# Optimization experiments

Hardware: AMD Instinct MI355X
Metric: run time of the kernel (lower is better)

## Reference

```python
import jax, jax.numpy as jnp
import numpy as np

B, N, F, T = 64, 1024, 8, 12
H, NLAYERS, K, OUT = 32, 3, 10, 12
E_RAND = N * 32


def setup_inputs() -> dict:
    key = jax.random.key(0)
    ks = jax.random.split(key, 11)
    x = jax.random.normal(ks[0], (B, N, F, T), jnp.float32)
    src = jax.random.randint(ks[1], (E_RAND,), 0, N)
    dst = jax.random.randint(ks[2], (E_RAND,), 0, N)
    loop = jnp.arange(N)
    edge_index = jnp.stack([jnp.concatenate([src, loop]),
                            jnp.concatenate([dst, loop])]).astype(jnp.int32)
    # weights in (0.1, 1.0) so all degrees are strictly positive
    edge_weight = jax.random.uniform(ks[3], (E_RAND + N,), jnp.float32, 0.1, 1.0)
    s = 0.1  # ~ 1/sqrt(H) init scale, matches torch defaults in spirit
    gru_w_ih = jax.random.normal(ks[4], (3 * H, F), jnp.float32) * s
    gru_w_hh = jax.random.normal(ks[5], (3 * H, H), jnp.float32) * s
    gru_b_ih = jax.random.normal(ks[6], (3 * H,), jnp.float32) * s
    gru_b_hh = jax.random.normal(ks[7], (3 * H,), jnp.float32) * s
    conv_w = jax.random.normal(ks[8], (NLAYERS, H, H), jnp.float32) * (1.0 / np.sqrt(H))
    lin_w = jax.random.normal(ks[9], (H, OUT), jnp.float32) * (1.0 / np.sqrt(H))
    lin_b = jax.random.normal(ks[10], (OUT,), jnp.float32) * s
    return {"x": x, "edge_index": edge_index, "edge_weight": edge_weight,
            "gru_w_ih": gru_w_ih, "gru_w_hh": gru_w_hh,
            "gru_b_ih": gru_b_ih, "gru_b_hh": gru_b_hh,
            "conv_w": conv_w, "lin_w": lin_w, "lin_b": lin_b}


def reference(x, edge_index, edge_weight, gru_w_ih, gru_w_hh, gru_b_ih, gru_b_hh,
              conv_w, lin_w, lin_b):
    Bsz, Nn, Fe, Tt = x.shape
    Hh = gru_w_hh.shape[1]

    # ---- temporal GRU over [B*N, T, F], keep last hidden state ----
    xt = jnp.transpose(x, (0, 1, 3, 2)).reshape(Bsz * Nn, Tt, Fe)
    gates_x = xt @ gru_w_ih.T + gru_b_ih  # [BN, T, 3H], input gates precomputed

    def step(h, gx):
        gh = h @ gru_w_hh.T + gru_b_hh
        xr, xz, xn = jnp.split(gx, 3, axis=-1)
        hr, hz, hn = jnp.split(gh, 3, axis=-1)
        r = jax.nn.sigmoid(xr + hr)
        z = jax.nn.sigmoid(xz + hz)
        n = jnp.tanh(xn + r * hn)
        return (1.0 - z) * n + z * h, None

    h0 = jnp.zeros((Bsz * Nn, Hh), x.dtype)
    hT, _ = jax.lax.scan(step, h0, jnp.swapaxes(gates_x, 0, 1))
    h = hT.reshape(Bsz, Nn, Hh)  # [B, N, H]

    # ---- normalized Laplacian (shared across batch) ----
    A = jnp.zeros((Nn, Nn), x.dtype).at[edge_index[0], edge_index[1]].add(edge_weight)
    d_isqrt = 1.0 / jnp.sqrt(A.sum(axis=1))  # row-degree, matches A.sum(dim=2)
    Lap = jnp.eye(Nn, dtype=x.dtype) - d_isqrt[:, None] * A * d_isqrt[None, :]

    # ---- rank-K spectral filter: M = U_k diag(S_k) U_k^T ----
    # torch code SVDs the identical L[b] per batch element; sign flips of U
    # columns cancel in U_k (.) U_k^T, so one SVD is mathematically identical.
    U, S, _ = jnp.linalg.svd(Lap, full_matrices=False)
    M = (U[:, :K] * S[:K]) @ U[:, :K].T  # [N, N]

    for w in conv_w:  # static 3-layer loop
        h = jax.nn.relu(jnp.einsum('nm,bmh,hk->bnk', M, h, w)) + h

    return h @ lin_w + lin_b  # [B, N, 12]
```

## Files before the change

### kernel.cpp

```cpp
#include <hip/hip_runtime.h>
#include <math.h>


#define NN 1024
#define PP 48
#define JSWEEPS 3

__global__ __launch_bounds__(256) void k_gru(
    const float* __restrict__ x, const float* __restrict__ wih,
    const float* __restrict__ whh, const float* __restrict__ bih,
    const float* __restrict__ bhh, float* __restrict__ hout) {
  __shared__ float s_x[64][97];
  __shared__ float s_h[64][33];
  int tid = threadIdx.x;
  int row = tid & 63;
  int i_base = __builtin_amdgcn_readfirstlane((tid >> 6) * 8);
  long row0 = (long)blockIdx.x * 64;

  for (int i = tid; i < 64 * 24; i += 256) {
    int r = i / 24, c = i % 24;
    float4 v = *(const float4*)&x[(row0 + r) * 96 + c * 4];
    s_x[r][c * 4 + 0] = v.x; s_x[r][c * 4 + 1] = v.y;
    s_x[r][c * 4 + 2] = v.z; s_x[r][c * 4 + 3] = v.w;
  }
  for (int i = tid; i < 64 * 32; i += 256) s_h[i / 32][i % 32] = 0.f;
  __syncthreads();

  float h[32];
#pragma unroll
  for (int k = 0; k < 32; ++k) h[k] = 0.f;

  for (int t = 0; t < 12; ++t) {
    float x8[8];
#pragma unroll
    for (int f = 0; f < 8; ++f) x8[f] = s_x[row][f * 12 + t];
    for (int ii = 0; ii < 8; ++ii) {
      int i = i_base + ii;
      float ar = bih[i] + bhh[i];
      float az = bih[32 + i] + bhh[32 + i];
      float gx = bih[64 + i];
      float gh = bhh[64 + i];
#pragma unroll
      for (int f = 0; f < 8; ++f) {
        ar += x8[f] * wih[i * 8 + f];
        az += x8[f] * wih[(32 + i) * 8 + f];
        gx += x8[f] * wih[(64 + i) * 8 + f];
      }
#pragma unroll
      for (int k = 0; k < 32; ++k) {
        ar += h[k] * whh[i * 32 + k];
        az += h[k] * whh[(32 + i) * 32 + k];
        gh += h[k] * whh[(64 + i) * 32 + k];
      }
      ar = fminf(fmaxf(ar, -30.f), 30.f);
      az = fminf(fmaxf(az, -30.f), 30.f);
      float r = __frcp_rn(1.f + __expf(-ar));
      float z = __frcp_rn(1.f + __expf(-az));
      float a = gx + r * gh;
      a = fminf(fmaxf(a, -15.f), 15.f);
      float e2 = __expf(2.f * a);
      float n = (e2 - 1.f) * __frcp_rn(e2 + 1.f);
      float hold = s_h[row][i];
      s_h[row][i] = (1.f - z) * n + z * hold;
    }
    __syncthreads();
#pragma unroll
    for (int k = 0; k < 32; ++k) h[k] = s_h[row][k];
    __syncthreads();
  }
  for (int idx = tid; idx < 64 * 8; idx += 256) {
    int r = idx >> 3, c4 = idx & 7;
    float4 v = make_float4(s_h[r][c4 * 4], s_h[r][c4 * 4 + 1],
                           s_h[r][c4 * 4 + 2], s_h[r][c4 * 4 + 3]);
    *(float4*)&hout[(row0 + r) * 32 + c4 * 4] = v;
  }
}

__global__ void k_scatter(const int* __restrict__ ei, const float* __restrict__ ew,
                          float* __restrict__ A, int E) {
  int e = blockIdx.x * 256 + threadIdx.x;
  if (e < E) atomicAdd(&A[ei[e] * NN + ei[E + e]], ew[e]);
}

__global__ __launch_bounds__(256) void k_degree(const float* __restrict__ A,
                                                float* __restrict__ disq) {
  __shared__ float red[256];
  int row = blockIdx.x, tid = threadIdx.x;
  float s = 0.f;
  for (int j = tid; j < NN; j += 256) s += A[row * NN + j];
  red[tid] = s;
  __syncthreads();
  for (int off = 128; off > 0; off >>= 1) {
    if (tid < off) red[tid] += red[tid + off];
    __syncthreads();
  }
  if (tid == 0) disq[row] = 1.f / sqrtf(red[0]);
}

__global__ void k_lap(float* __restrict__ A, const float* __restrict__ disq) {
  int idx = blockIdx.x * 256 + threadIdx.x;
  int i = idx >> 10, j = idx & 1023;
  float v = -disq[i] * A[idx] * disq[j];
  if (i == j) v += 1.f;
  A[idx] = v;
}

__global__ __launch_bounds__(256) void k_mm_sym(const float* __restrict__ A,
                                                float* __restrict__ C) {
  if (blockIdx.x < blockIdx.y) return;
  __shared__ float As[32][68];
  __shared__ float Bs[32][68];
  __shared__ float Ts[64][65];
  int tid = threadIdx.x;
  int tx = tid & 15, ty = tid >> 4;
  int i0 = blockIdx.y * 64, j0 = blockIdx.x * 64;
  float acc[4][4];
#pragma unroll
  for (int a = 0; a < 4; ++a)
#pragma unroll
    for (int b = 0; b < 4; ++b) acc[a][b] = 0.f;
  int lrow = tid >> 3;
  int kk0 = (tid & 7) * 4;
  float4 pa0 = *(const float4*)&A[(long)(i0 + lrow) * NN + kk0];
  float4 pa1 = *(const float4*)&A[(long)(i0 + lrow + 32) * NN + kk0];
  float4 pb0 = *(const float4*)&A[(long)(j0 + lrow) * NN + kk0];
  float4 pb1 = *(const float4*)&A[(long)(j0 + lrow + 32) * NN + kk0];
  for (int k0 = 0; k0 < NN; k0 += 32) {
    As[kk0 + 0][lrow] = pa0.x; As[kk0 + 1][lrow] = pa0.y;
    As[kk0 + 2][lrow] = pa0.z; As[kk0 + 3][lrow] = pa0.w;
    As[kk0 + 0][lrow + 32] = pa1.x; As[kk0 + 1][lrow + 32] = pa1.y;
    As[kk0 + 2][lrow + 32] = pa1.z; As[kk0 + 3][lrow + 32] = pa1.w;
    Bs[kk0 + 0][lrow] = pb0.x; Bs[kk0 + 1][lrow] = pb0.y;
    Bs[kk0 + 2][lrow] = pb0.z; Bs[kk0 + 3][lrow] = pb0.w;
    Bs[kk0 + 0][lrow + 32] = pb1.x; Bs[kk0 + 1][lrow + 32] = pb1.y;
    Bs[kk0 + 2][lrow + 32] = pb1.z; Bs[kk0 + 3][lrow + 32] = pb1.w;
    __syncthreads();
    if (k0 + 32 < NN) {
      pa0 = *(const float4*)&A[(long)(i0 + lrow) * NN + k0 + 32 + kk0];
      pa1 = *(const float4*)&A[(long)(i0 + lrow + 32) * NN + k0 + 32 + kk0];
      pb0 = *(const float4*)&A[(long)(j0 + lrow) * NN + k0 + 32 + kk0];
      pb1 = *(const float4*)&A[(long)(j0 + lrow + 32) * NN + k0 + 32 + kk0];
    }
#pragma unroll
    for (int kk = 0; kk < 32; ++kk) {
      float4 av = *(const float4*)&As[kk][ty * 4];
      float4 bv = *(const float4*)&Bs[kk][tx * 4];
      float aa[4] = {av.x, av.y, av.z, av.w};
      float bb[4] = {bv.x, bv.y, bv.z, bv.w};
#pragma unroll
      for (int a = 0; a < 4; ++a)
#pragma unroll
        for (int b = 0; b < 4; ++b) acc[a][b] += aa[a] * bb[b];
    }
    __syncthreads();
  }
#pragma unroll
  for (int a = 0; a < 4; ++a) {
    float4 v = make_float4(acc[a][0], acc[a][1], acc[a][2], acc[a][3]);
    *(float4*)&C[(long)(i0 + ty * 4 + a) * NN + j0 + tx * 4] = v;
  }
  if (i0 != j0) {
#pragma unroll
    for (int a = 0; a < 4; ++a)
#pragma unroll
      for (int b = 0; b < 4; ++b)
        Ts[tx * 4 + b][ty * 4 + a] = acc[a][b];
    __syncthreads();
    for (int idx = tid; idx < 64 * 16; idx += 256) {
      int r = idx >> 4, c4 = idx & 15;
      float4 v = make_float4(Ts[r][c4 * 4], Ts[r][c4 * 4 + 1],
                             Ts[r][c4 * 4 + 2], Ts[r][c4 * 4 + 3]);
      *(float4*)&C[(long)(j0 + r) * NN + i0 + c4 * 4] = v;
    }
  }
}

__global__ void k_q0(float* __restrict__ Q) {
  int i = blockIdx.x * 256 + threadIdx.x;
  if (i < NN * PP) {
    unsigned u = (unsigned)i * 2654435761u;
    u ^= u >> 16; u *= 2246822519u; u ^= u >> 13; u *= 3266489917u; u ^= u >> 16;
    Q[i] = (float)(u & 0xFFFFFF) * (1.f / 16777216.f) - 0.5f;
  }
}

__global__ __launch_bounds__(256) void k_spmm(const float* __restrict__ Gp,
                                              const float* __restrict__ Q,
                                              float* __restrict__ Zp) {
  __shared__ float Qs[64][49];
  __shared__ float Gs[16][65];
  int tid = threadIdx.x;
  int r = tid >> 4;
  int c0 = (tid & 15) * 3;
  int row0 = blockIdx.x * 16;
  int k0 = blockIdx.y * 256;
  float a0 = 0.f, a1 = 0.f, a2 = 0.f;
  for (int kt = 0; kt < 4; ++kt) {
    int kb = k0 + kt * 64;
    for (int idx = tid; idx < 64 * PP; idx += 256) {
      int qr = idx / PP, qc = idx % PP;
      Qs[qr][qc] = Q[(kb + qr) * PP + qc];
    }
    for (int idx = tid; idx < 16 * 64; idx += 256) {
      int gr = idx >> 6, gk = idx & 63;
      Gs[gr][gk] = Gp[(long)(row0 + gr) * NN + kb + gk];
    }
    __syncthreads();
#pragma unroll 4
    for (int kk = 0; kk < 64; ++kk) {
      float g = Gs[r][kk];
      a0 += g * Qs[kk][c0];
      a1 += g * Qs[kk][c0 + 1];
      a2 += g * Qs[kk][c0 + 2];
    }
    __syncthreads();
  }
  float* zp = Zp + (long)blockIdx.y * (NN * PP);
  zp[(row0 + r) * PP + c0] = a0;
  zp[(row0 + r) * PP + c0 + 1] = a1;
  zp[(row0 + r) * PP + c0 + 2] = a2;
}

__global__ __launch_bounds__(256) void k_gram(const float* __restrict__ Zp,
                                              float* __restrict__ Z,
                                              float* __restrict__ Sp) {
  __shared__ float Zs[32][49];
  int tid = threadIdx.x;
  int r0 = blockIdx.x * 32;
  for (int idx = tid; idx < 32 * PP; idx += 256) {
    int r = idx / PP, c = idx % PP;
    long g = (long)(r0 + r) * PP + c;
    float s = Zp[g] + Zp[g + NN * PP] + Zp[g + 2 * NN * PP] + Zp[g + 3 * NN * PP];
    Zs[r][c] = s;
    Z[g] = s;
  }
  __syncthreads();
  float* sp = Sp + blockIdx.x * (PP * PP);
  for (int cell = tid; cell < PP * PP; cell += 256) {
    int i = cell / PP, j = cell % PP;
    float a = 0.f;
#pragma unroll 8
    for (int r = 0; r < 32; ++r) a += Zs[r][i] * Zs[r][j];
    sp[cell] = a;
  }
}

__global__ __launch_bounds__(256) void k_tbuild(const float* __restrict__ Qa,
                                                const float* __restrict__ Zp,
                                                float* __restrict__ Tp) {
  __shared__ float Qs[32][49];
  __shared__ float Ys[32][49];
  int tid = threadIdx.x;
  int r0 = blockIdx.x * 32;
  for (int idx = tid; idx < 32 * PP; idx += 256) {
    int r = idx / PP, c = idx % PP;
    long g = (long)(r0 + r) * PP + c;
    Qs[r][c] = Qa[g];
    Ys[r][c] = Zp[g] + Zp[g + NN * PP] + Zp[g + 2 * NN * PP] + Zp[g + 3 * NN * PP];
  }
  __syncthreads();
  float* tp = Tp + blockIdx.x * (PP * PP);
  for (int cell = tid; cell < PP * PP; cell += 256) {
    int i = cell / PP, j = cell % PP;
    float a = 0.f;
#pragma unroll 8
    for (int r = 0; r < 32; ++r) a += Qs[r][i] * Ys[r][j];
    tp[cell] = a;
  }
}

__global__ __launch_bounds__(256) void k_qr(const float* __restrict__ Sp,
                                            float* __restrict__ Q) {
  __shared__ float R[PP][PP + 1];
  __shared__ float rs[PP];
  __shared__ float idiag[PP];
  int tid = threadIdx.x;
  for (int idx = tid; idx < PP * PP; idx += 256) {
    float s = 0.f;
    for (int b = 0; b < 32; ++b) s += Sp[b * (PP * PP) + idx];
    R[idx / PP][idx % PP] = s;
  }
  __syncthreads();
  for (int j = 0; j < PP; ++j) {
    float d = R[j][j];
    float sq = sqrtf(d > 1e-30f ? d : 1e-30f);
    float invd = 1.f / sq;
    for (int c = j + tid; c < PP; c += 256)
      rs[c] = (c == j) ? sq : R[j][c] * invd;
    __syncthreads();
    int m = PP - 1 - j;
    for (int idx = tid; idx < m * m; idx += 256) {
      int i = j + 1 + idx / m, c = j + 1 + idx % m;
      R[i][c] -= rs[i] * rs[c];
    }
    for (int c = j + tid; c < PP; c += 256) R[j][c] = rs[c];
    __syncthreads();
  }
  if (tid < PP) idiag[tid] = 1.f / R[tid][tid];
  __syncthreads();
  int row = blockIdx.x * 256 + tid;
  float q[PP];
#pragma unroll
  for (int k = 0; k < PP; ++k) q[k] = Q[row * PP + k];
#pragma unroll
  for (int c = 0; c < PP; ++c) {
    float s = q[c];
#pragma unroll
    for (int k = 0; k < c; ++k) s -= q[k] * R[k][c];
    q[c] = s * idiag[c];
  }
#pragma unroll
  for (int k = 0; k < PP; ++k) Q[row * PP + k] = q[k];
}

__global__ __launch_bounds__(384) void k_jacobi(const float* __restrict__ Tp,
                                                float* __restrict__ Vsel,
                                                float* __restrict__ s10) {
  __shared__ float Ta[PP][PP + 1], Tb[PP][PP + 1];
  __shared__ float Va[PP][PP + 1], Vb[PP][PP + 1];
  __shared__ float w0[PP], w1[PP];
  __shared__ int j0a[PP], j1a[PP];
  __shared__ int selidx[10];
  int tid = threadIdx.x;
  for (int idx = tid; idx < PP * PP; idx += 384) {
    float s = 0.f;
    for (int b = 0; b < 32; ++b) s += Tp[b * (PP * PP) + idx];
    Tb[idx / PP][idx % PP] = s;
  }
  __syncthreads();
  for (int idx = tid; idx < PP * PP; idx += 384) {
    int i = idx / PP, j = idx % PP;
    Ta[i][j] = 0.5f * (Tb[i][j] + Tb[j][i]);
    Va[i][j] = (i == j) ? 1.f : 0.f;
  }
  __syncthreads();
  float (*Tc)[PP + 1] = Ta, (*Tn)[PP + 1] = Tb;
  float (*Vc)[PP + 1] = Va, (*Vn)[PP + 1] = Vb;
  int i_row = tid >> 3;
  int jb = (tid & 7) * 6;
  for (int sweep = 0; sweep < JSWEEPS; ++sweep) {
    for (int r = 0; r < PP - 1; ++r) {
      if (tid < 24) {
        int k = tid;
        int p = (k == 0) ? 0 : ((r + k - 1) % 47) + 1;
        int q = ((r + 46 - k) % 47) + 1;
        float app = Tc[p][p], aqq = Tc[q][q], apq = Tc[p][q];
        float c = 1.f, s = 0.f;
        if (fabsf(apq) > 1e-30f) {
          float tau = (aqq - app) / (2.f * apq);
          float den = fabsf(tau) + sqrtf(1.f + tau * tau);
          float tt = copysignf(1.f / den, tau);
          c = 1.f / sqrtf(1.f + tt * tt);
          s = tt * c;
        }
        j0a[p] = p; j1a[p] = q; w0[p] = c;  w1[p] = -s;
        j0a[q] = p; j1a[q] = q; w0[q] = s;  w1[q] = c;
      }
      __syncthreads();
      float wi0 = w0[i_row], wi1 = w1[i_row];
      int i0 = j0a[i_row], i1 = j1a[i_row];
      float tnew[6], vnew[6];
#pragma unroll
      for (int m = 0; m < 6; ++m) {
        int j = jb + m;
        float wj0 = w0[j], wj1 = w1[j];
        int a = j0a[j], b = j1a[j];
        tnew[m] = wi0 * (wj0 * Tc[i0][a] + wj1 * Tc[i0][b]) +
                  wi1 * (wj0 * Tc[i1][a] + wj1 * Tc[i1][b]);
        vnew[m] = wj0 * Vc[i_row][a] + wj1 * Vc[i_row][b];
      }
#pragma unroll
      for (int m = 0; m < 6; ++m) {
        Tn[i_row][jb + m] = tnew[m];
        Vn[i_row][jb + m] = vnew[m];
      }
      __syncthreads();
      float (*tt_)[PP + 1] = Tc; Tc = Tn; Tn = tt_;
      float (*vt_)[PP + 1] = Vc; Vc = Vn; Vn = vt_;
    }
  }
  if (tid < 64) {
    float v = (tid < PP) ? Tc[tid][tid] : -1e30f;
    for (int sel = 0; sel < 10; ++sel) {
      float bv = v; int bi = tid;
      for (int off = 32; off > 0; off >>= 1) {
        float ov = __shfl_xor(bv, off);
        int oi = __shfl_xor(bi, off);
        if (ov > bv || (ov == bv && oi < bi)) { bv = ov; bi = oi; }
      }
      if (tid == 0) { selidx[sel] = bi; s10[sel] = sqrtf(fmaxf(bv, 0.f)); }
      if (tid == bi) v = -1e30f;
    }
  }
  __syncthreads();
  for (int idx = tid; idx < PP * 10; idx += 384) {
    int j = idx / 10, i = idx % 10;
    Vsel[idx] = Vc[j][selidx[i]];
  }
}

__global__ __launch_bounds__(256) void k_u10(const float* __restrict__ Q,
                                             const float* __restrict__ Vsel,
                                             float* __restrict__ U10) {
  __shared__ float Vs[PP * 10];
  int tid = threadIdx.x;
  for (int idx = tid; idx < PP * 10; idx += 256) Vs[idx] = Vsel[idx];
  __syncthreads();
  int row = blockIdx.x * 256 + tid;
  float q[PP];
#pragma unroll
  for (int k = 0; k < PP; ++k) q[k] = Q[row * PP + k];
#pragma unroll
  for (int i = 0; i < 10; ++i) {
    float s = 0.f;
#pragma unroll
    for (int k = 0; k < PP; ++k) s += q[k] * Vs[k * 10 + i];
    U10[row * 10 + i] = s;
  }
}

__global__ __launch_bounds__(320) void k_p0w(const float* __restrict__ h,
                                             const float* __restrict__ U10,
                                             const float* __restrict__ W,
                                             const float* __restrict__ s10,
                                             float* __restrict__ P1) {
  __shared__ float Hs[128][33];
  __shared__ float Us[128][10];
  __shared__ float P0s[10][33];
  __shared__ float Ws[32][32];
  int tid = threadIdx.x;
  int b = blockIdx.x;
  int i = tid / 32, kk = tid % 32;
  for (int idx = tid; idx < 1024; idx += 320) Ws[idx / 32][idx % 32] = W[idx];
  float acc = 0.f;
  for (int t0 = 0; t0 < NN; t0 += 128) {
    for (int idx = tid; idx < 128 * 32; idx += 320) {
      int r = idx / 32, c = idx % 32;
      Hs[r][c] = h[(long)(b * NN + t0 + r) * 32 + c];
    }
    for (int idx = tid; idx < 1280; idx += 320)
      Us[idx / 10][idx % 10] = U10[(t0 + idx / 10) * 10 + idx % 10];
    __syncthreads();
#pragma unroll 8
    for (int r = 0; r < 128; ++r) acc += Us[r][i] * Hs[r][kk];
    __syncthreads();
  }
  P0s[i][kk] = acc;
  __syncthreads();
  float a = 0.f;
#pragma unroll
  for (int j = 0; j < 32; ++j) a += P0s[i][j] * Ws[j][kk];
  P1[b * 320 + i * 32 + kk] = s10[i] * a;
}

template <int LAST>
__global__ __launch_bounds__(256) void k_update(float* __restrict__ h,
                                                const float* __restrict__ U10,
                                                const float* __restrict__ P1,
                                                const float* __restrict__ lw,
                                                const float* __restrict__ lb,
                                                float* __restrict__ out) {
  __shared__ float a1[10][32];
  __shared__ float Us[64][10];
  __shared__ float hl[64][33];
  int tid = threadIdx.x;
  int b = blockIdx.x, n0 = blockIdx.y * 64;
  for (int idx = tid; idx < 320; idx += 256)
    a1[idx / 32][idx % 32] = P1[b * 320 + idx];
  for (int idx = tid; idx < 640; idx += 256)
    Us[idx / 10][idx % 10] = U10[(n0 + idx / 10) * 10 + idx % 10];
  __syncthreads();
  for (int idx = tid; idx < 2048; idx += 256) {
    int nl = idx / 32, k = idx % 32;
    float z = 0.f;
#pragma unroll
    for (int i = 0; i < 10; ++i) z += Us[nl][i] * a1[i][k];
    long g = (long)(b * NN + n0 + nl) * 32 + k;
    float hn = h[g] + fmaxf(z, 0.f);
    if (LAST) hl[nl][k] = hn;
    else h[g] = hn;
  }
  if (LAST) {
    __syncthreads();
    for (int idx = tid; idx < 64 * 12; idx += 256) {
      int row = idx / 12, o = idx % 12;
      float s = lb[o];
#pragma unroll
      for (int j = 0; j < 32; ++j) s += hl[row][j] * lw[j * 12 + o];
      out[(long)(b * NN + n0 + row) * 12 + o] = s;
    }
  }
}

extern "C" void kernel_launch(void* const* d_in, const int* in_sizes, int n_in,
                              void* d_out, int out_size, void* d_ws, size_t ws_size,
                              hipStream_t stream) {
  const float* x    = (const float*)d_in[0];
  const int*   ei   = (const int*)d_in[1];
  const float* ew   = (const float*)d_in[2];
  const float* wih  = (const float*)d_in[3];
  const float* whh  = (const float*)d_in[4];
  const float* bih  = (const float*)d_in[5];
  const float* bhh  = (const float*)d_in[6];
  const float* convw = (const float*)d_in[7];
  const float* lw   = (const float*)d_in[8];
  const float* lb   = (const float*)d_in[9];
  float* out = (float*)d_out;
  float* ws  = (float*)d_ws;
  int E = in_sizes[1] / 2;

  float* h    = ws;
  float* B1   = h + 2097152;
  float* B2   = B1 + 1048576;
  float* B3   = B2 + 1048576;
  float* Qa   = B3 + 1048576;
  float* Qb   = Qa + 49152;
  float* Zp   = Qb + 49152;
  float* Sp   = Zp + 196608;
  float* Tp   = Sp + 73728;
  float* Vsel = Tp + 73728;
  float* s10  = Vsel + 480;
  float* U10  = s10 + 16;
  float* P1   = U10 + 10240;
  float* disq = P1 + 20480;

  k_gru<<<1024, 256, 0, stream>>>(x, wih, whh, bih, bhh, h);

  hipMemsetAsync(B1, 0, (size_t)1048576 * 4, stream);
  k_scatter<<<(E + 255) / 256, 256, 0, stream>>>(ei, ew, B1, E);
  k_degree<<<NN, 256, 0, stream>>>(B1, disq);
  k_lap<<<4096, 256, 0, stream>>>(B1, disq);
  k_mm_sym<<<dim3(16, 16), 256, 0, stream>>>(B1, B2);
  k_mm_sym<<<dim3(16, 16), 256, 0, stream>>>(B2, B3);
  k_mm_sym<<<dim3(16, 16), 256, 0, stream>>>(B3, B1);
  k_mm_sym<<<dim3(16, 16), 256, 0, stream>>>(B1, B3);
  k_mm_sym<<<dim3(16, 16), 256, 0, stream>>>(B3, B1);
  k_mm_sym<<<dim3(16, 16), 256, 0, stream>>>(B1, B3);

  k_q0<<<192, 256, 0, stream>>>(Qa);
  for (int it = 0; it < 6; ++it) {
    float* src = (it & 1) ? Qb : Qa;
    float* dst = (it & 1) ? Qa : Qb;
    k_spmm<<<dim3(64, 4), 256, 0, stream>>>(B3, src, Zp);
    k_gram<<<32, 256, 0, stream>>>(Zp, dst, Sp);
    k_qr<<<4, 256, 0, stream>>>(Sp, dst);
  }

  k_spmm<<<dim3(64, 4), 256, 0, stream>>>(B2, Qa, Zp);
  k_tbuild<<<32, 256, 0, stream>>>(Qa, Zp, Tp);
  k_jacobi<<<1, 384, 0, stream>>>(Tp, Vsel, s10);
  k_u10<<<4, 256, 0, stream>>>(Qa, Vsel, U10);

  for (int l = 0; l < 3; ++l) {
    k_p0w<<<64, 320, 0, stream>>>(h, U10, convw + l * 1024, s10, P1);
    if (l < 2)
      k_update<0><<<dim3(64, 16), 256, 0, stream>>>(h, U10, P1, lw, lb, out);
    else
      k_update<1><<<dim3(64, 16), 256, 0, stream>>>(h, U10, P1, lw, lb, out);
  }
}
```

Before: 1.270 ms.

## Split-K matrix powers, fuse Laplacian build, pipeline Jacobi coefficients, split P0 reduction

The symmetric 1024x1024 matrix-power products drop the half-grid triangle trick and run as a full grid with a two-way split over K, followed by a fold kernel. This raises block count from 136 active to 512. The Laplacian normalisation moves into the first product's tile load, which removes the separate k_lap pass. The single-block Jacobi eigensolver adds a warp that computes the next round's rotation coefficients while the other threads apply the current rotation, halving the barriers per round. The per-layer U^T h reduction is split across four blocks per batch element, with the W multiply moved into the update kernel. The GRU launch moves after the spectral stage so the h buffer can serve as split-K scratch. The costs are extra global traffic for the partials and the fold, and redundant W multiplies in every update block.

Result: faster. 1.130 ms (-11.1%).

```diff
diff --git a/kernel.cpp b/kernel.cpp
--- a/kernel.cpp
+++ b/kernel.cpp
@@ -5,6 +5,7 @@
 #define NN 1024
 #define PP 48
 #define JSWEEPS 3
+#define NROUNDS (JSWEEPS * (PP - 1))
 
 __global__ __launch_bounds__(256) void k_gru(
     const float* __restrict__ x, const float* __restrict__ wih,
@@ -97,23 +98,16 @@
   if (tid == 0) disq[row] = 1.f / sqrtf(red[0]);
 }
 
-__global__ void k_lap(float* __restrict__ A, const float* __restrict__ disq) {
-  int idx = blockIdx.x * 256 + threadIdx.x;
-  int i = idx >> 10, j = idx & 1023;
-  float v = -disq[i] * A[idx] * disq[j];
-  if (i == j) v += 1.f;
-  A[idx] = v;
-}
-
-__global__ __launch_bounds__(256) void k_mm_sym(const float* __restrict__ A,
-                                                float* __restrict__ C) {
-  if (blockIdx.x < blockIdx.y) return;
+template <int LAP>
+__global__ __launch_bounds__(256) void k_mmsplit(const float* __restrict__ A,
+                                                 const float* __restrict__ disq,
+                                                 float* __restrict__ Cp) {
   __shared__ float As[32][68];
   __shared__ float Bs[32][68];
-  __shared__ float Ts[64][65];
   int tid = threadIdx.x;
   int tx = tid & 15, ty = tid >> 4;
   int i0 = blockIdx.y * 64, j0 = blockIdx.x * 64;
+  int kbase = blockIdx.z * 512;
   float acc[4][4];
 #pragma unroll
   for (int a = 0; a < 4; ++a)
@@ -121,21 +115,43 @@
     for (int b = 0; b < 4; ++b) acc[a][b] = 0.f;
   int lrow = tid >> 3;
   int kk0 = (tid & 7) * 4;
-  float4 pa0 = *(const float4*)&A[(long)(i0 + lrow) * NN + kk0];
-  float4 pa1 = *(const float4*)&A[(long)(i0 + lrow + 32) * NN + kk0];
-  float4 pb0 = *(const float4*)&A[(long)(j0 + lrow) * NN + kk0];
-  float4 pb1 = *(const float4*)&A[(long)(j0 + lrow + 32) * NN + kk0];
-  for (int k0 = 0; k0 < NN; k0 += 32) {
-    As[kk0 + 0][lrow] = pa0.x; As[kk0 + 1][lrow] = pa0.y;
-    As[kk0 + 2][lrow] = pa0.z; As[kk0 + 3][lrow] = pa0.w;
-    As[kk0 + 0][lrow + 32] = pa1.x; As[kk0 + 1][lrow + 32] = pa1.y;
-    As[kk0 + 2][lrow + 32] = pa1.z; As[kk0 + 3][lrow + 32] = pa1.w;
-    Bs[kk0 + 0][lrow] = pb0.x; Bs[kk0 + 1][lrow] = pb0.y;
-    Bs[kk0 + 2][lrow] = pb0.z; Bs[kk0 + 3][lrow] = pb0.w;
-    Bs[kk0 + 0][lrow + 32] = pb1.x; Bs[kk0 + 1][lrow + 32] = pb1.y;
-    Bs[kk0 + 2][lrow + 32] = pb1.z; Bs[kk0 + 3][lrow + 32] = pb1.w;
-    __syncthreads();
-    if (k0 + 32 < NN) {
+  float drA0 = 0.f, drA1 = 0.f, drB0 = 0.f, drB1 = 0.f;
+  if (LAP) {
+    drA0 = disq[i0 + lrow]; drA1 = disq[i0 + lrow + 32];
+    drB0 = disq[j0 + lrow]; drB1 = disq[j0 + lrow + 32];
+  }
+  float4 pa0 = *(const float4*)&A[(long)(i0 + lrow) * NN + kbase + kk0];
+  float4 pa1 = *(const float4*)&A[(long)(i0 + lrow + 32) * NN + kbase + kk0];
+  float4 pb0 = *(const float4*)&A[(long)(j0 + lrow) * NN + kbase + kk0];
+  float4 pb1 = *(const float4*)&A[(long)(j0 + lrow + 32) * NN + kbase + kk0];
+  for (int k0 = kbase; k0 < kbase + 512; k0 += 32) {
+    if (LAP) {
+      float4 dq = *(const float4*)&disq[k0 + kk0];
+      int kg = k0 + kk0;
+#pragma unroll
+      for (int e = 0; e < 4; ++e) {
+        float dqe = (e == 0) ? dq.x : (e == 1) ? dq.y : (e == 2) ? dq.z : dq.w;
+        float a0e = (e == 0) ? pa0.x : (e == 1) ? pa0.y : (e == 2) ? pa0.z : pa0.w;
+        float a1e = (e == 0) ? pa1.x : (e == 1) ? pa1.y : (e == 2) ? pa1.z : pa1.w;
+        float b0e = (e == 0) ? pb0.x : (e == 1) ? pb0.y : (e == 2) ? pb0.z : pb0.w;
+        float b1e = (e == 0) ? pb1.x : (e == 1) ? pb1.y : (e == 2) ? pb1.z : pb1.w;
+        As[kk0 + e][lrow]      = -drA0 * a0e * dqe + ((i0 + lrow == kg + e) ? 1.f : 0.f);
+        As[kk0 + e][lrow + 32] = -drA1 * a1e * dqe + ((i0 + lrow + 32 == kg + e) ? 1.f : 0.f);
+        Bs[kk0 + e][lrow]      = -drB0 * b0e * dqe + ((j0 + lrow == kg + e) ? 1.f : 0.f);
+        Bs[kk0 + e][lrow + 32] = -drB1 * b1e * dqe + ((j0 + lrow + 32 == kg + e) ? 1.f : 0.f);
+      }
+    } else {
+      As[kk0 + 0][lrow] = pa0.x; As[kk0 + 1][lrow] = pa0.y;
+      As[kk0 + 2][lrow] = pa0.z; As[kk0 + 3][lrow] = pa0.w;
+      As[kk0 + 0][lrow + 32] = pa1.x; As[kk0 + 1][lrow + 32] = pa1.y;
+      As[kk0 + 2][lrow + 32] = pa1.z; As[kk0 + 3][lrow + 32] = pa1.w;
+      Bs[kk0 + 0][lrow] = pb0.x; Bs[kk0 + 1][lrow] = pb0.y;
+      Bs[kk0 + 2][lrow] = pb0.z; Bs[kk0 + 3][lrow] = pb0.w;
+      Bs[kk0 + 0][lrow + 32] = pb1.x; Bs[kk0 + 1][lrow + 32] = pb1.y;
+      Bs[kk0 + 2][lrow + 32] = pb1.z; Bs[kk0 + 3][lrow + 32] = pb1.w;
+    }
+    __syncthreads();
+    if (k0 + 32 < kbase + 512) {
       pa0 = *(const float4*)&A[(long)(i0 + lrow) * NN + k0 + 32 + kk0];
       pa1 = *(const float4*)&A[(long)(i0 + lrow + 32) * NN + k0 + 32 + kk0];
       pb0 = *(const float4*)&A[(long)(j0 + lrow) * NN + k0 + 32 + kk0];
@@ -154,25 +170,21 @@
     }
     __syncthreads();
   }
+  float* cp = Cp + (long)blockIdx.z * (NN * NN);
 #pragma unroll
   for (int a = 0; a < 4; ++a) {
     float4 v = make_float4(acc[a][0], acc[a][1], acc[a][2], acc[a][3]);
-    *(float4*)&C[(long)(i0 + ty * 4 + a) * NN + j0 + tx * 4] = v;
-  }
-  if (i0 != j0) {
-#pragma unroll
-    for (int a = 0; a < 4; ++a)
-#pragma unroll
-      for (int b = 0; b < 4; ++b)
-        Ts[tx * 4 + b][ty * 4 + a] = acc[a][b];
-    __syncthreads();
-    for (int idx = tid; idx < 64 * 16; idx += 256) {
-      int r = idx >> 4, c4 = idx & 15;
-      float4 v = make_float4(Ts[r][c4 * 4], Ts[r][c4 * 4 + 1],
-                             Ts[r][c4 * 4 + 2], Ts[r][c4 * 4 + 3]);
-      *(float4*)&C[(long)(j0 + r) * NN + i0 + c4 * 4] = v;
-    }
-  }
+    *(float4*)&cp[(long)(i0 + ty * 4 + a) * NN + j0 + tx * 4] = v;
+  }
+}
+
+__global__ __launch_bounds__(256) void k_fold(const float* __restrict__ Cp,
+                                              float* __restrict__ C) {
+  int i = (blockIdx.x * 256 + threadIdx.x) * 4;
+  float4 a = *(const float4*)&Cp[i];
+  float4 b = *(const float4*)&Cp[i + NN * NN];
+  float4 v = make_float4(a.x + b.x, a.y + b.y, a.z + b.z, a.w + b.w);
+  *(float4*)&C[i] = v;
 }
 
 __global__ void k_q0(float* __restrict__ Q) {
@@ -313,58 +325,77 @@
   for (int k = 0; k < PP; ++k) Q[row * PP + k] = q[k];
 }
 
-__global__ __launch_bounds__(384) void k_jacobi(const float* __restrict__ Tp,
+__global__ __launch_bounds__(448) void k_jacobi(const float* __restrict__ Tp,
                                                 float* __restrict__ Vsel,
                                                 float* __restrict__ s10) {
   __shared__ float Ta[PP][PP + 1], Tb[PP][PP + 1];
   __shared__ float Va[PP][PP + 1], Vb[PP][PP + 1];
-  __shared__ float w0[PP], w1[PP];
-  __shared__ int j0a[PP], j1a[PP];
+  __shared__ float w0b[2][PP], w1b[2][PP];
+  __shared__ int j0b[2][PP], j1b[2][PP];
   __shared__ int selidx[10];
   int tid = threadIdx.x;
-  for (int idx = tid; idx < PP * PP; idx += 384) {
+  for (int idx = tid; idx < PP * PP; idx += 448) {
     float s = 0.f;
     for (int b = 0; b < 32; ++b) s += Tp[b * (PP * PP) + idx];
     Tb[idx / PP][idx % PP] = s;
   }
   __syncthreads();
-  for (int idx = tid; idx < PP * PP; idx += 384) {
+  for (int idx = tid; idx < PP * PP; idx += 448) {
     int i = idx / PP, j = idx % PP;
     Ta[i][j] = 0.5f * (Tb[i][j] + Tb[j][i]);
     Va[i][j] = (i == j) ? 1.f : 0.f;
   }
+  if (tid < PP) {
+    j0b[0][tid] = tid; j1b[0][tid] = tid;
+    w0b[0][tid] = 1.f; w1b[0][tid] = 0.f;
+  }
   __syncthreads();
   float (*Tc)[PP + 1] = Ta, (*Tn)[PP + 1] = Tb;
   float (*Vc)[PP + 1] = Va, (*Vn)[PP + 1] = Vb;
+
+  auto coeff_phase = [&](int rr, int cur, int nxt,
+                         float (*Tcur)[PP + 1]) {
+    int k = tid - 384;
+    int P = (k == 0) ? 0 : ((rr + k - 1) % 47) + 1;
+    int Q = ((rr + 46 - k) % 47) + 1;
+    int P0 = j0b[cur][P], P1 = j1b[cur][P];
+    float Pw0 = w0b[cur][P], Pw1 = w1b[cur][P];
+    int Q0 = j0b[cur][Q], Q1 = j1b[cur][Q];
+    float Qw0 = w0b[cur][Q], Qw1 = w1b[cur][Q];
+    float app = Pw0 * (Pw0 * Tcur[P0][P0] + Pw1 * Tcur[P0][P1]) +
+                Pw1 * (Pw0 * Tcur[P1][P0] + Pw1 * Tcur[P1][P1]);
+    float apq = Pw0 * (Qw0 * Tcur[P0][Q0] + Qw1 * Tcur[P0][Q1]) +
+                Pw1 * (Qw0 * Tcur[P1][Q0] + Qw1 * Tcur[P1][Q1]);
+    float aqq = Qw0 * (Qw0 * Tcur[Q0][Q0] + Qw1 * Tcur[Q0][Q1]) +
+                Qw1 * (Qw0 * Tcur[Q1][Q0] + Qw1 * Tcur[Q1][Q1]);
+    float c = 1.f, s = 0.f;
+    if (fabsf(apq) > 1e-30f) {
+      float tau = (aqq - app) / (2.f * apq);
+      float den = fabsf(tau) + sqrtf(1.f + tau * tau);
+      float tt = copysignf(1.f / den, tau);
+      c = 1.f / sqrtf(1.f + tt * tt);
+      s = tt * c;
+    }
+    j0b[nxt][P] = P; j1b[nxt][P] = Q; w0b[nxt][P] = c;  w1b[nxt][P] = -s;
+    j0b[nxt][Q] = P; j1b[nxt][Q] = Q; w0b[nxt][Q] = s;  w1b[nxt][Q] = c;
+  };
+
+  if (tid >= 384 && tid < 408) coeff_phase(0, 0, 1, Tc);
+  __syncthreads();
+
+  int cur = 1;
   int i_row = tid >> 3;
   int jb = (tid & 7) * 6;
-  for (int sweep = 0; sweep < JSWEEPS; ++sweep) {
-    for (int r = 0; r < PP - 1; ++r) {
-      if (tid < 24) {
-        int k = tid;
-        int p = (k == 0) ? 0 : ((r + k - 1) % 47) + 1;
-        int q = ((r + 46 - k) % 47) + 1;
-        float app = Tc[p][p], aqq = Tc[q][q], apq = Tc[p][q];
-        float c = 1.f, s = 0.f;
-        if (fabsf(apq) > 1e-30f) {
-          float tau = (aqq - app) / (2.f * apq);
-          float den = fabsf(tau) + sqrtf(1.f + tau * tau);
-          float tt = copysignf(1.f / den, tau);
-          c = 1.f / sqrtf(1.f + tt * tt);
-          s = tt * c;
-        }
-        j0a[p] = p; j1a[p] = q; w0[p] = c;  w1[p] = -s;
-        j0a[q] = p; j1a[q] = q; w0[q] = s;  w1[q] = c;
-      }
-      __syncthreads();
-      float wi0 = w0[i_row], wi1 = w1[i_row];
-      int i0 = j0a[i_row], i1 = j1a[i_row];
+  for (int R = 0; R < NROUNDS; ++R) {
+    if (tid < 384) {
+      float wi0 = w0b[cur][i_row], wi1 = w1b[cur][i_row];
+      int i0 = j0b[cur][i_row], i1 = j1b[cur][i_row];
       float tnew[6], vnew[6];
 #pragma unroll
       for (int m = 0; m < 6; ++m) {
         int j = jb + m;
-        float wj0 = w0[j], wj1 = w1[j];
-        int a = j0a[j], b = j1a[j];
+        float wj0 = w0b[cur][j], wj1 = w1b[cur][j];
+        int a = j0b[cur][j], b = j1b[cur][j];
         tnew[m] = wi0 * (wj0 * Tc[i0][a] + wj1 * Tc[i0][b]) +
                   wi1 * (wj0 * Tc[i1][a] + wj1 * Tc[i1][b]);
         vnew[m] = wj0 * Vc[i_row][a] + wj1 * Vc[i_row][b];
@@ -374,11 +405,15 @@
         Tn[i_row][jb + m] = tnew[m];
         Vn[i_row][jb + m] = vnew[m];
       }
-      __syncthreads();
-      float (*tt_)[PP + 1] = Tc; Tc = Tn; Tn = tt_;
-      float (*vt_)[PP + 1] = Vc; Vc = Vn; Vn = vt_;
-    }
-  }
+    } else if (tid < 408 && R + 1 < NROUNDS) {
+      coeff_phase((R + 1) % 47, cur, cur ^ 1, Tc);
+    }
+    __syncthreads();
+    float (*tt_)[PP + 1] = Tc; Tc = Tn; Tn = tt_;
+    float (*vt_)[PP + 1] = Vc; Vc = Vn; Vn = vt_;
+    cur ^= 1;
+  }
+
   if (tid < 64) {
     float v = (tid < PP) ? Tc[tid][tid] : -1e30f;
     for (int sel = 0; sel < 10; ++sel) {
@@ -393,7 +428,7 @@
     }
   }
   __syncthreads();
-  for (int idx = tid; idx < PP * 10; idx += 384) {
+  for (int idx = tid; idx < PP * 10; idx += 448) {
     int j = idx / 10, i = idx % 10;
     Vsel[idx] = Vc[j][selidx[i]];
   }
@@ -419,62 +454,68 @@
   }
 }
 
-__global__ __launch_bounds__(320) void k_p0w(const float* __restrict__ h,
-                                             const float* __restrict__ U10,
-                                             const float* __restrict__ W,
-                                             const float* __restrict__ s10,
-                                             float* __restrict__ P1) {
+__global__ __launch_bounds__(320) void k_p0(const float* __restrict__ h,
+                                            const float* __restrict__ U10,
+                                            float* __restrict__ Pp) {
   __shared__ float Hs[128][33];
   __shared__ float Us[128][10];
-  __shared__ float P0s[10][33];
-  __shared__ float Ws[32][32];
-  int tid = threadIdx.x;
-  int b = blockIdx.x;
+  int tid = threadIdx.x;
+  int b = blockIdx.x >> 2, ch = blockIdx.x & 3;
   int i = tid / 32, kk = tid % 32;
-  for (int idx = tid; idx < 1024; idx += 320) Ws[idx / 32][idx % 32] = W[idx];
+  int base = ch * 256;
   float acc = 0.f;
-  for (int t0 = 0; t0 < NN; t0 += 128) {
+  for (int t0 = 0; t0 < 256; t0 += 128) {
     for (int idx = tid; idx < 128 * 32; idx += 320) {
       int r = idx / 32, c = idx % 32;
-      Hs[r][c] = h[(long)(b * NN + t0 + r) * 32 + c];
+      Hs[r][c] = h[(long)(b * NN + base + t0 + r) * 32 + c];
     }
     for (int idx = tid; idx < 1280; idx += 320)
-      Us[idx / 10][idx % 10] = U10[(t0 + idx / 10) * 10 + idx % 10];
+      Us[idx / 10][idx % 10] = U10[(base + t0 + idx / 10) * 10 + idx % 10];
     __syncthreads();
 #pragma unroll 8
     for (int r = 0; r < 128; ++r) acc += Us[r][i] * Hs[r][kk];
     __syncthreads();
   }
-  P0s[i][kk] = acc;
-  __syncthreads();
-  float a = 0.f;
-#pragma unroll
-  for (int j = 0; j < 32; ++j) a += P0s[i][j] * Ws[j][kk];
-  P1[b * 320 + i * 32 + kk] = s10[i] * a;
+  Pp[(long)blockIdx.x * 320 + tid] = acc;
 }
 
 template <int LAST>
 __global__ __launch_bounds__(256) void k_update(float* __restrict__ h,
                                                 const float* __restrict__ U10,
-                                                const float* __restrict__ P1,
+                                                const float* __restrict__ Pp,
+                                                const float* __restrict__ W,
+                                                const float* __restrict__ s10,
                                                 const float* __restrict__ lw,
                                                 const float* __restrict__ lb,
                                                 float* __restrict__ out) {
-  __shared__ float a1[10][32];
+  __shared__ float P0s[10][32];
+  __shared__ float P1s[10][32];
+  __shared__ float Ws[32][32];
   __shared__ float Us[64][10];
   __shared__ float hl[64][33];
   int tid = threadIdx.x;
   int b = blockIdx.x, n0 = blockIdx.y * 64;
-  for (int idx = tid; idx < 320; idx += 256)
-    a1[idx / 32][idx % 32] = P1[b * 320 + idx];
+  for (int idx = tid; idx < 320; idx += 256) {
+    long g = (long)b * 4 * 320 + idx;
+    P0s[idx / 32][idx % 32] = Pp[g] + Pp[g + 320] + Pp[g + 640] + Pp[g + 960];
+  }
+  for (int idx = tid; idx < 1024; idx += 256) Ws[idx / 32][idx % 32] = W[idx];
   for (int idx = tid; idx < 640; idx += 256)
     Us[idx / 10][idx % 10] = U10[(n0 + idx / 10) * 10 + idx % 10];
+  __syncthreads();
+  for (int idx = tid; idx < 320; idx += 256) {
+    int i = idx / 32, kk = idx % 32;
+    float a = 0.f;
+#pragma unroll
+    for (int j = 0; j < 32; ++j) a += P0s[i][j] * Ws[j][kk];
+    P1s[i][kk] = s10[i] * a;
+  }
   __syncthreads();
   for (int idx = tid; idx < 2048; idx += 256) {
     int nl = idx / 32, k = idx % 32;
     float z = 0.f;
 #pragma unroll
-    for (int i = 0; i < 10; ++i) z += Us[nl][i] * a1[i][k];
+    for (int i = 0; i < 10; ++i) z += Us[nl][i] * P1s[i][k];
     long g = (long)(b * NN + n0 + nl) * 32 + k;
     float hn = h[g] + fmaxf(z, 0.f);
     if (LAST) hl[nl][k] = hn;
@@ -521,21 +562,25 @@
   float* Vsel = Tp + 73728;
   float* s10  = Vsel + 480;
   float* U10  = s10 + 16;
-  float* P1   = U10 + 10240;
-  float* disq = P1 + 20480;
-
-  k_gru<<<1024, 256, 0, stream>>>(x, wih, whh, bih, bhh, h);
+  float* disq = U10 + 10240;
+  float* Pp   = Zp;
+  float* Cp   = h;
 
   hipMemsetAsync(B1, 0, (size_t)1048576 * 4, stream);
   k_scatter<<<(E + 255) / 256, 256, 0, stream>>>(ei, ew, B1, E);
   k_degree<<<NN, 256, 0, stream>>>(B1, disq);
-  k_lap<<<4096, 256, 0, stream>>>(B1, disq);
-  k_mm_sym<<<dim3(16, 16), 256, 0, stream>>>(B1, B2);
-  k_mm_sym<<<dim3(16, 16), 256, 0, stream>>>(B2, B3);
-  k_mm_sym<<<dim3(16, 16), 256, 0, stream>>>(B3, B1);
-  k_mm_sym<<<dim3(16, 16), 256, 0, stream>>>(B1, B3);
-  k_mm_sym<<<dim3(16, 16), 256, 0, stream>>>(B3, B1);
-  k_mm_sym<<<dim3(16, 16), 256, 0, stream>>>(B1, B3);
+  k_mmsplit<1><<<dim3(16, 16, 2), 256, 0, stream>>>(B1, disq, Cp);
+  k_fold<<<1024, 256, 0, stream>>>(Cp, B2);
+  k_mmsplit<0><<<dim3(16, 16, 2), 256, 0, stream>>>(B2, disq, Cp);
+  k_fold<<<1024, 256, 0, stream>>>(Cp, B3);
+  k_mmsplit<0><<<dim3(16, 16, 2), 256, 0, stream>>>(B3, disq, Cp);
+  k_fold<<<1024, 256, 0, stream>>>(Cp, B1);
+  k_mmsplit<0><<<dim3(16, 16, 2), 256, 0, stream>>>(B1, disq, Cp);
+  k_fold<<<1024, 256, 0, stream>>>(Cp, B3);
+  k_mmsplit<0><<<dim3(16, 16, 2), 256, 0, stream>>>(B3, disq, Cp);
+  k_fold<<<1024, 256, 0, stream>>>(Cp, B1);
+  k_mmsplit<0><<<dim3(16, 16, 2), 256, 0, stream>>>(B1, disq, Cp);
+  k_fold<<<1024, 256, 0, stream>>>(Cp, B3);
 
   k_q0<<<192, 256, 0, stream>>>(Qa);
   for (int it = 0; it < 6; ++it) {
@@ -548,14 +593,18 @@
 
   k_spmm<<<dim3(64, 4), 256, 0, stream>>>(B2, Qa, Zp);
   k_tbuild<<<32, 256, 0, stream>>>(Qa, Zp, Tp);
-  k_jacobi<<<1, 384, 0, stream>>>(Tp, Vsel, s10);
+  k_jacobi<<<1, 448, 0, stream>>>(Tp, Vsel, s10);
   k_u10<<<4, 256, 0, stream>>>(Qa, Vsel, U10);
 
+  k_gru<<<1024, 256, 0, stream>>>(x, wih, whh, bih, bhh, h);
+
   for (int l = 0; l < 3; ++l) {
-    k_p0w<<<64, 320, 0, stream>>>(h, U10, convw + l * 1024, s10, P1);
+    k_p0<<<256, 320, 0, stream>>>(h, U10, Pp);
     if (l < 2)
-      k_update<0><<<dim3(64, 16), 256, 0, stream>>>(h, U10, P1, lw, lb, out);
+      k_update<0><<<dim3(64, 16), 256, 0, stream>>>(h, U10, Pp, convw + l * 1024,
+                                                    s10, lw, lb, out);
     else
-      k_update<1><<<dim3(64, 16), 256, 0, stream>>>(h, U10, P1, lw, lb, out);
-  }
-}
+      k_update<1><<<dim3(64, 16), 256, 0, stream>>>(h, U10, Pp, convw + l * 1024,
+                                                    s10, lw, lb, out);
+  }
+}
```
